# Kernel tuning notes

Hardware: AMD Instinct MI355X
Metric: run time of the kernel (lower is better)

The kernel has to match this reference:

```python
import jax, jax.numpy as jnp
import numpy as np

N_EMBD = 1024
N_HEAD = 16


def setup_inputs() -> dict:
    key = jax.random.key(0)
    ks = jax.random.split(key, 11)
    B, T, T2, C = 4, 2048, 1024, N_EMBD
    s = 0.02
    return {
        "x": jax.random.normal(ks[0], (B, T, C), jnp.float32),
        "enc_x": jax.random.normal(ks[1], (B, T2, C), jnp.float32),
        "Wq": jax.random.normal(ks[2], (C, C), jnp.float32) * s,
        "bq": jax.random.normal(ks[3], (C,), jnp.float32) * s,
        "Wk": jax.random.normal(ks[4], (C, C), jnp.float32) * s,
        "bk": jax.random.normal(ks[5], (C,), jnp.float32) * s,
        "Wv": jax.random.normal(ks[6], (C, C), jnp.float32) * s,
        "bv": jax.random.normal(ks[7], (C,), jnp.float32) * s,
        "Wo": jax.random.normal(ks[8], (C, C), jnp.float32) * s,
        "bo": jax.random.normal(ks[9], (C,), jnp.float32) * s,
    }


def reference(x, enc_x, Wq, bq, Wk, bk, Wv, bv, Wo, bo):
    B, T, C = x.shape
    B2, T2, C2 = enc_x.shape
    H = N_HEAD
    D = C // H  # head dim
    q = x @ Wq + bq          # [B,T,C]
    k = enc_x @ Wk + bk      # [B,T2,C]
    v = enc_x @ Wv + bv      # [B,T2,C]
    q = q.reshape(B, T, H, D).transpose(0, 2, 1, 3)    # [B,H,T,D]
    k = k.reshape(B2, T2, H, D).transpose(0, 2, 1, 3)  # [B,H,T2,D]
    v = v.reshape(B2, T2, H, D).transpose(0, 2, 1, 3)  # [B,H,T2,D]
    att = jnp.einsum("bhtd,bhsd->bhts", q, k) * (1.0 / jnp.sqrt(jnp.float32(D)))
    att = jax.nn.softmax(att, axis=-1)                 # [B,H,T,T2]
    y = jnp.einsum("bhts,bhsd->bhtd", att, v)          # [B,H,T,D]
    y = y.transpose(0, 2, 1, 3).reshape(B, T, C)
    return y @ Wo + bo
```

## Files before the change

### kernel.cpp

```cpp
#include <hip/hip_runtime.h>
#include <hip/hip_bf16.h>


typedef __bf16 bf16_t;
typedef __bf16 bf16x8 __attribute__((ext_vector_type(8)));
typedef float f32x4 __attribute__((ext_vector_type(4)));
typedef float f32x16 __attribute__((ext_vector_type(16)));
typedef unsigned int u32x4 __attribute__((ext_vector_type(4)));

#define AS1C(p) ((const __attribute__((address_space(1))) void*)(p))
#define AS3(p)  ((__attribute__((address_space(3))) void*)(p))

constexpr int CC  = 1024;
constexpr int TT  = 2048;
constexpr int TT2 = 1024;

#if __has_builtin(__builtin_amdgcn_exp2f)
__device__ __forceinline__ float EXP2(float x) { return __builtin_amdgcn_exp2f(x); }
#else
__device__ __forceinline__ float EXP2(float x) { return exp2f(x); }
#endif

__global__ void cast2(const float* __restrict__ in0, bf16_t* __restrict__ out0, int n0,
                      const float* __restrict__ in1, bf16_t* __restrict__ out1, int n1) {
    int i = blockIdx.x * blockDim.x + threadIdx.x;
    int stride = gridDim.x * blockDim.x;
    for (; i < n0 + n1; i += stride) {
        const float* in = (i < n0) ? in0 : in1;
        bf16_t* out = (i < n0) ? out0 : out1;
        int j = (i < n0) ? i : i - n0;
        const float4* p = (const float4*)in + 2 * (size_t)j;
        float4 a = p[0], b = p[1];
        bf16x8 v;
        v[0] = (bf16_t)a.x; v[1] = (bf16_t)a.y; v[2] = (bf16_t)a.z; v[3] = (bf16_t)a.w;
        v[4] = (bf16_t)b.x; v[5] = (bf16_t)b.y; v[6] = (bf16_t)b.z; v[7] = (bf16_t)b.w;
        *(bf16x8*)(out + (size_t)j * 8) = v;
    }
}

__global__ __launch_bounds__(256) void transW(const float* __restrict__ W0, const float* __restrict__ W1,
                                              const float* __restrict__ W2, const float* __restrict__ W3,
                                              bf16_t* __restrict__ T0, bf16_t* __restrict__ T1,
                                              bf16_t* __restrict__ T2, bf16_t* __restrict__ T3) {
    __shared__ float tile[32][33];
    const float* W; bf16_t* Tt;
    switch (blockIdx.z) {
        case 0:  W = W0; Tt = T0; break;
        case 1:  W = W1; Tt = T1; break;
        case 2:  W = W2; Tt = T2; break;
        default: W = W3; Tt = T3; break;
    }
    int x = threadIdx.x & 31, y = threadIdx.x >> 5;
    int bx = blockIdx.x * 32, by = blockIdx.y * 32;
    for (int i = 0; i < 4; ++i) {
        int r = y + i * 8;
        tile[r][x] = W[(size_t)(by + r) * 1024 + bx + x];
    }
    __syncthreads();
    for (int i = 0; i < 4; ++i) {
        int r = y + i * 8;
        Tt[(size_t)(bx + r) * 1024 + by + x] = (bf16_t)tile[x][r];
    }
}


#define SB0 __builtin_amdgcn_sched_barrier(0)
#define GLL(src, dst) __builtin_amdgcn_global_load_lds(AS1C(src), AS3(dst), 16, 0, 0)

__device__ __forceinline__ bf16x8 ldx(const char* p) { return *(const bf16x8*)p; }

__global__ __launch_bounds__(512, 2) void gemm_qkv8(const bf16_t* __restrict__ xb,
                                                    const bf16_t* __restrict__ eb,
                                                    const bf16_t* __restrict__ wtq,
                                                    const bf16_t* __restrict__ wtk,
                                                    const float* __restrict__ bq,
                                                    const float* __restrict__ bk,
                                                    const float* __restrict__ bv,
                                                    bf16_t* __restrict__ Qs,
                                                    bf16_t* __restrict__ Ks,
                                                    bf16_t* __restrict__ Vs,
                                                    float qscale) {
    __shared__ __align__(16) char GLDS[131072];
    char* ldsA = &GLDS[0];
    char* ldsB = &GLDS[65536];

    const int tid = threadIdx.x;
    const int w   = tid >> 6;
    const int l   = tid & 63;
    const int wm  = w >> 2;
    const int wn  = w & 3;
    const int l15 = l & 15, lhi = l >> 4;

    const int bid = blockIdx.x;
    const bf16_t* Ap; const bf16_t* Bp;
    int m0, n0;
    float scale;
    const float* bias; bf16_t* outp; int outn0;
    if (bid < 128) {
        int xcd = bid & 7, j = bid >> 3;
        n0 = (j & 3) * 256; m0 = (xcd * 4 + (j >> 2)) * 256;
        Ap = xb; Bp = wtq; scale = qscale;
        bias = bq; outp = Qs; outn0 = n0;
    } else {
        int b2 = bid - 128;
        int xcd = b2 & 7, j = b2 >> 3;
        n0 = (j & 7) * 256; m0 = (xcd * 2 + (j >> 3)) * 256;
        Ap = eb; Bp = wtk; scale = 1.0f;
        if (n0 < 1024) { bias = bk; outp = Ks; outn0 = n0; }
        else           { bias = bv; outp = Vs; outn0 = n0 - 1024; }
    }

    const int lrow  = l >> 3;
    const int lslot = (l & 7) ^ lrow;
    const char* Asrc = (const char*)(Ap + (size_t)(m0 + w * 16 + lrow) * 1024 + lslot * 8);
    const char* Bsrc = (const char*)(Bp + (size_t)(n0 + w * 16 + lrow) * 1024 + lslot * 8);
    #define STG_A(t, buf, h)                                                                   \
        do {                                                                                   \
            GLL(Asrc + (size_t)(h) * 262144 + (t) * 128,         ldsA + (buf) * 32768 + (h) * 16384 + w * 2048);        \
            GLL(Asrc + (size_t)(h) * 262144 + 16384 + (t) * 128, ldsA + (buf) * 32768 + (h) * 16384 + w * 2048 + 1024); \
        } while (0)
    #define STG_B(t, buf, h)                                                                   \
        do {                                                                                   \
            GLL(Bsrc + (size_t)(h) * 262144 + (t) * 128,         ldsB + (buf) * 32768 + (h) * 16384 + w * 2048);        \
            GLL(Bsrc + (size_t)(h) * 262144 + 16384 + (t) * 128, ldsB + (buf) * 32768 + (h) * 16384 + w * 2048 + 1024); \
        } while (0)

    const int aoff = (wm * 128 + l15) * 128;
    const int boff = (wn * 64 + l15) * 128;
    const int sl0  = ((0 + lhi) ^ (l15 & 7)) << 4;
    const int sl1  = ((4 + lhi) ^ (l15 & 7)) << 4;

    #define RD_A(dst, KA, qm)                                                    \
        do { _Pragma("unroll") for (int mf = 0; mf < 4; ++mf) {                  \
            dst[mf * 2 + 0] = ldx((KA) + aoff + ((qm) * 64 + mf * 16) * 128 + sl0); \
            dst[mf * 2 + 1] = ldx((KA) + aoff + ((qm) * 64 + mf * 16) * 128 + sl1); } } while (0)
    #define RD_B(dst, KB, qn)                                                    \
        do { _Pragma("unroll") for (int nf = 0; nf < 2; ++nf) {                  \
            dst[nf * 2 + 0] = ldx((KB) + boff + ((qn) * 32 + nf * 16) * 128 + sl0); \
            dst[nf * 2 + 1] = ldx((KB) + boff + ((qn) * 32 + nf * 16) * 128 + sl1); } } while (0)

    #define MFMA16(qm, qn, Af, Bf)                                                             \
        do { __builtin_amdgcn_s_setprio(1);                                                    \
            _Pragma("unroll") for (int mf = 0; mf < 4; ++mf)                                   \
            _Pragma("unroll") for (int nf = 0; nf < 2; ++nf) {                                 \
                acc[(qm) * 4 + mf][(qn) * 2 + nf] = __builtin_amdgcn_mfma_f32_16x16x32_bf16(   \
                    Af[mf * 2 + 0], Bf[nf * 2 + 0], acc[(qm) * 4 + mf][(qn) * 2 + nf], 0, 0, 0); \
                acc[(qm) * 4 + mf][(qn) * 2 + nf] = __builtin_amdgcn_mfma_f32_16x16x32_bf16(   \
                    Af[mf * 2 + 1], Bf[nf * 2 + 1], acc[(qm) * 4 + mf][(qn) * 2 + nf], 0, 0, 0); } \
            __builtin_amdgcn_s_setprio(0); } while (0)

    #define PH_BAR do { SB0; __builtin_amdgcn_s_barrier(); SB0;                                \
                        asm volatile("s_waitcnt lgkmcnt(0)" ::: "memory"); SB0; } while (0)
    #define PH_END do { SB0; __builtin_amdgcn_s_barrier(); SB0; } while (0)

    f32x4 acc[8][4] = {};
    bf16x8 A0[8], A1[8], B0[4], B1[4];

    STG_A(0, 0, 0); STG_A(0, 0, 1);
    STG_B(0, 0, 0); STG_B(0, 0, 1);
    STG_A(1, 1, 0); STG_A(1, 1, 1);
    asm volatile("s_waitcnt vmcnt(4)" ::: "memory");
    SB0; __builtin_amdgcn_s_barrier(); SB0;

    constexpr int NT = 16;
    for (int t = 0; t < NT; ++t) {
        const int buf = t & 1;
        const char* KA = ldsA + buf * 32768;
        const char* KB = ldsB + buf * 32768;

        if (t + 1 < NT) STG_B(t + 1, buf ^ 1, 0);
        RD_A(A0, KA, 0); RD_B(B0, KB, 0);
        PH_BAR;
        MFMA16(0, 0, A0, B0);
        PH_END;

        if (t + 1 < NT) STG_B(t + 1, buf ^ 1, 1);
        RD_A(A1, KA, 1);
        PH_BAR;
        MFMA16(1, 0, A1, B0);
        PH_END;

        if (t + 2 < NT) STG_A(t + 2, buf, 0);
        RD_B(B1, KB, 1);
        PH_BAR;
        MFMA16(1, 1, A1, B1);
        PH_END;

        if (t + 2 < NT) STG_A(t + 2, buf, 1);
        SB0; __builtin_amdgcn_s_barrier(); SB0;
        MFMA16(0, 1, A0, B1);
        if (t < NT - 2) asm volatile("s_waitcnt vmcnt(4)" ::: "memory");
        else            asm volatile("s_waitcnt vmcnt(0)" ::: "memory");
        PH_END;
    }

    #pragma unroll
    for (int ni = 0; ni < 4; ++ni) {
        int col = outn0 + wn * 64 + ni * 16 + l15;
        float bvv = bias[col];
        #pragma unroll
        for (int mi = 0; mi < 8; ++mi) {
            int rowb = m0 + wm * 128 + mi * 16 + lhi * 4;
            #pragma unroll
            for (int r = 0; r < 4; ++r)
                outp[(size_t)(rowb + r) * 1024 + col] = (bf16_t)((acc[mi][ni][r] + bvv) * scale);
        }
    }
    #undef STG_A
    #undef STG_B
    #undef RD_A
    #undef RD_B
    #undef MFMA16
    #undef PH_BAR
    #undef PH_END
}

__device__ __forceinline__ void gemm_body(bf16_t* As, bf16_t* Bs,
                                          const bf16_t* __restrict__ A,
                                          const bf16_t* __restrict__ Bt,
                                          const float* __restrict__ bias,
                                          float* __restrict__ out,
                                          int lgNT, int mband, int bid) {
    const int tid  = threadIdx.x;
    const int lane = tid & 63;
    const int wave = tid >> 6;
    const int wr = wave >> 1, wc = wave & 1;
    const int l15 = lane & 15, lhi = lane >> 4;

    const int xcd = bid & 7;
    const int j   = bid >> 3;
    const int n0  = (j & ((1 << lgNT) - 1)) * 128;
    const int m0  = (xcd * mband + (j >> lgNT)) * 128;

    f32x4 acc[4][4] = {};

    for (int k0 = 0; k0 < 1024; k0 += 32) {
        for (int i = 0; i < 2; ++i) {
            int e   = i * 2048 + wave * 512 + lane * 8;
            int row = e >> 5, col = e & 31;
            __builtin_amdgcn_global_load_lds(AS1C(A  + (size_t)(m0 + row) * 1024 + k0 + col),
                                             AS3(As + i * 2048 + wave * 512), 16, 0, 0);
            __builtin_amdgcn_global_load_lds(AS1C(Bt + (size_t)(n0 + row) * 1024 + k0 + col),
                                             AS3(Bs + i * 2048 + wave * 512), 16, 0, 0);
        }
        __syncthreads();
        bf16x8 a[4], b[4];
        #pragma unroll
        for (int m = 0; m < 4; ++m)
            a[m] = *(const bf16x8*)&As[(wr * 64 + m * 16 + l15) * 32 + lhi * 8];
        #pragma unroll
        for (int n = 0; n < 4; ++n)
            b[n] = *(const bf16x8*)&Bs[(wc * 64 + n * 16 + l15) * 32 + lhi * 8];
        #pragma unroll
        for (int m = 0; m < 4; ++m)
            #pragma unroll
            for (int n = 0; n < 4; ++n)
                acc[m][n] = __builtin_amdgcn_mfma_f32_16x16x32_bf16(a[m], b[n], acc[m][n], 0, 0, 0);
        __syncthreads();
    }

    #pragma unroll
    for (int n = 0; n < 4; ++n) {
        int col = n0 + wc * 64 + n * 16 + l15;
        float bv = bias[col];
        #pragma unroll
        for (int m = 0; m < 4; ++m) {
            int rowb = m0 + wr * 64 + m * 16 + lhi * 4;
            #pragma unroll
            for (int r = 0; r < 4; ++r)
                out[(size_t)(rowb + r) * 1024 + col] = acc[m][n][r] + bv;
        }
    }
}

__global__ __launch_bounds__(256) void gemm_out(const bf16_t* __restrict__ yb,
                                                const bf16_t* __restrict__ wto,
                                                const float* __restrict__ bo,
                                                float* __restrict__ out) {
    __shared__ __align__(16) bf16_t As[128 * 32];
    __shared__ __align__(16) bf16_t Bs[128 * 32];
    gemm_body(As, Bs, yb, wto, bo, out, 3, 8, blockIdx.x);
}

__global__ __launch_bounds__(256) void vtrans(const bf16_t* __restrict__ Vs, bf16_t* __restrict__ Vt) {
    __shared__ bf16_t t[64][72];
    int bh = blockIdx.y, b = bh >> 4, h = bh & 15;
    int kv0 = blockIdx.x * 64;
    int r = threadIdx.x >> 2, c0 = (threadIdx.x & 3) * 16;
    const bf16_t* src = Vs + (size_t)(b * 1024 + kv0 + r) * 1024 + h * 64 + c0;
    *(bf16x8*)&t[r][c0]     = *(const bf16x8*)src;
    *(bf16x8*)&t[r][c0 + 8] = *(const bf16x8*)(src + 8);
    __syncthreads();
    int d = threadIdx.x >> 2, k0 = (threadIdx.x & 3) * 16;
    bf16x8 v0, v1;
    #pragma unroll
    for (int j = 0; j < 8; ++j) { v0[j] = t[k0 + j][d]; v1[j] = t[k0 + 8 + j][d]; }
    bf16_t* dst = Vt + ((size_t)bh * 64 + d) * 1024 + kv0 + k0;
    *(bf16x8*)dst       = v0;
    *(bf16x8*)(dst + 8) = v1;
}

__device__ __forceinline__ unsigned pk_bf16(float lo, float hi) {
    unsigned r;
    asm("v_cvt_pk_bf16_f32 %0, %1, %2" : "=v"(r) : "v"(lo), "v"(hi));
    return r;
}
__device__ __forceinline__ void swap32(unsigned &a, unsigned &b) {
    asm("v_permlane32_swap_b32 %0, %1" : "+v"(a), "+v"(b));
}
__device__ __forceinline__ float sum_halves(float x) {
    unsigned a = __builtin_bit_cast(unsigned, x), b = a;
    swap32(a, b);
    return __builtin_bit_cast(float, a) + __builtin_bit_cast(float, b);
}
__device__ __forceinline__ bf16x8 ldsf(const bf16_t* base, int row, int colb) {
    int off = row * 128 + (colb ^ ((row & 7) << 4));
    return *(const bf16x8*)((const char*)base + off);
}
__device__ __forceinline__ bf16x8 packP(const f32x16& s0, const f32x16& s1, int kt) {
    const f32x16& sp = (kt < 2) ? s0 : s1;
    const int rb = (kt & 1) * 8;
    unsigned a0 = pk_bf16(sp[rb + 0], sp[rb + 1]);
    unsigned a1 = pk_bf16(sp[rb + 2], sp[rb + 3]);
    unsigned a2 = pk_bf16(sp[rb + 4], sp[rb + 5]);
    unsigned a3 = pk_bf16(sp[rb + 6], sp[rb + 7]);
    swap32(a0, a2);
    swap32(a1, a3);
    union { u32x4 u; bf16x8 h; } cv;
    cv.u = (u32x4){a0, a1, a2, a3};
    return cv.h;
}

__global__ __launch_bounds__(256, 2) void attn256(const bf16_t* __restrict__ Q,
                                                  const bf16_t* __restrict__ K,
                                                  const bf16_t* __restrict__ Vt,
                                                  bf16_t* __restrict__ Y) {
    __shared__ __align__(16) bf16_t SM[3][2][64 * 64];

    const int tid = threadIdx.x;
    const int l   = tid & 63;
    const int w   = tid >> 6;
    const int l31 = l & 31;
    const int lh  = l >> 5;

    const int bid = blockIdx.x;
    const int bh  = bid & 63;
    const int qb  = bid >> 6;
    const int b = bh >> 4, h = bh & 15;
    const int q0 = qb * 256 + w * 64;

    const bf16_t* Qb = Q + (size_t)b * TT * CC + h * 64;
    const char* Kc = (const char*)(K + (size_t)b * TT2 * CC + h * 64);
    const char* Vc = (const char*)(Vt + (size_t)bh * 64 * 1024);

    bf16x8 qfA[4], qfB[4];
    #pragma unroll
    for (int kt = 0; kt < 4; ++kt) {
        qfA[kt] = *(const bf16x8*)&Qb[(size_t)(q0 + l31)      * CC + kt * 16 + lh * 8];
        qfB[kt] = *(const bf16x8*)&Qb[(size_t)(q0 + 32 + l31) * CC + kt * 16 + lh * 8];
    }
    __builtin_amdgcn_sched_barrier(0);

    f32x16 yA0 = {}, yA1 = {}, yB0 = {}, yB1 = {};
    float lsA = 0.f, lsB = 0.f;

    const int krow = w * 16 + (l >> 3);
    const int ss   = ((l & 7) ^ (l >> 3)) & 7;
    const int off0 = krow * 2048 + ss * 16;
    const int off1 = off0 + 8 * 2048;

    #define STAGE(t, buf)                                                                 \
        do {                                                                              \
            __builtin_amdgcn_global_load_lds(AS1C(Kc + (size_t)(t) * 131072 + off0),      \
                                             AS3((char*)&SM[buf][0][0] + w * 2048), 16, 0, 0);        \
            __builtin_amdgcn_global_load_lds(AS1C(Kc + (size_t)(t) * 131072 + off1),      \
                                             AS3((char*)&SM[buf][0][0] + w * 2048 + 1024), 16, 0, 0); \
            __builtin_amdgcn_global_load_lds(AS1C(Vc + (t) * 128 + off0),                 \
                                             AS3((char*)&SM[buf][1][0] + w * 2048), 16, 0, 0);        \
            __builtin_amdgcn_global_load_lds(AS1C(Vc + (t) * 128 + off1),                 \
                                             AS3((char*)&SM[buf][1][0] + w * 2048 + 1024), 16, 0, 0); \
        } while (0)

    #define SUMEXP(s0, s1, ls)                                                    \
        do {                                                                      \
            float rs = 0.f;                                                       \
            _Pragma("unroll")                                                     \
            for (int r = 0; r < 16; ++r) {                                        \
                s0[r] = EXP2(s0[r]);                                              \
                s1[r] = EXP2(s1[r]);                                              \
                rs += s0[r] + s1[r];                                              \
            }                                                                     \
            ls += sum_halves(rs);                                                 \
        } while (0)

    constexpr int NT = TT2 / 64;
    STAGE(0, 0);
    STAGE(1, 1);

    int cur = 0;
    for (int t = 0; t < NT; ++t) {
        if (t + 1 < NT) asm volatile("s_waitcnt vmcnt(4)" ::: "memory");
        else            asm volatile("s_waitcnt vmcnt(0)" ::: "memory");
        __builtin_amdgcn_sched_barrier(0);
        __builtin_amdgcn_s_barrier();
        __builtin_amdgcn_sched_barrier(0);

        if (t + 2 < NT) {
            int nb = cur + 2; if (nb >= 3) nb -= 3;
            STAGE(t + 2, nb);
        }

        const bf16_t* Kl = &SM[cur][0][0];
        const bf16_t* Vl = &SM[cur][1][0];

        f32x16 sA0 = {}, sA1 = {}, sB0 = {}, sB1 = {};
        #pragma unroll
        for (int kt = 0; kt < 4; ++kt) {
            int colb = kt * 32 + (lh << 4);
            bf16x8 a0 = ldsf(Kl, l31,      colb);
            bf16x8 a1 = ldsf(Kl, 32 + l31, colb);
            sA0 = __builtin_amdgcn_mfma_f32_32x32x16_bf16(a0, qfA[kt], sA0, 0, 0, 0);
            sB0 = __builtin_amdgcn_mfma_f32_32x32x16_bf16(a0, qfB[kt], sB0, 0, 0, 0);
            sA1 = __builtin_amdgcn_mfma_f32_32x32x16_bf16(a1, qfA[kt], sA1, 0, 0, 0);
            sB1 = __builtin_amdgcn_mfma_f32_32x32x16_bf16(a1, qfB[kt], sB1, 0, 0, 0);
        }

        SUMEXP(sA0, sA1, lsA);
        SUMEXP(sB0, sB1, lsB);

        __builtin_amdgcn_s_setprio(1);
        #pragma unroll
        for (int kt = 0; kt < 4; ++kt) {
            bf16x8 pA = packP(sA0, sA1, kt);
            bf16x8 pB = packP(sB0, sB1, kt);
            int colb = kt * 32 + (lh << 4);
            bf16x8 v0 = ldsf(Vl, l31,      colb);
            bf16x8 v1 = ldsf(Vl, 32 + l31, colb);
            yA0 = __builtin_amdgcn_mfma_f32_32x32x16_bf16(v0, pA, yA0, 0, 0, 0);
            yA1 = __builtin_amdgcn_mfma_f32_32x32x16_bf16(v1, pA, yA1, 0, 0, 0);
            yB0 = __builtin_amdgcn_mfma_f32_32x32x16_bf16(v0, pB, yB0, 0, 0, 0);
            yB1 = __builtin_amdgcn_mfma_f32_32x32x16_bf16(v1, pB, yB1, 0, 0, 0);
        }
        __builtin_amdgcn_s_setprio(0);

        ++cur; if (cur == 3) cur = 0;
    }
    #undef STAGE
    #undef SUMEXP

    __syncthreads();

    float iA = 1.f / lsA, iB = 1.f / lsB;
    char* ob = (char*)&SM[0][0][0] + w * 8192;
    const int sw = (l31 & 7) << 4;
    #pragma unroll
    for (int r = 0; r < 16; ++r) {
        int drow = (r & 3) + 8 * (r >> 2) + 4 * lh;
        *(bf16_t*)(ob + l31 * 128 + ((drow * 2) ^ sw))               = (bf16_t)(yA0[r] * iA);
        *(bf16_t*)(ob + l31 * 128 + (((32 + drow) * 2) ^ sw))        = (bf16_t)(yA1[r] * iA);
        *(bf16_t*)(ob + 4096 + l31 * 128 + ((drow * 2) ^ sw))        = (bf16_t)(yB0[r] * iB);
        *(bf16_t*)(ob + 4096 + l31 * 128 + (((32 + drow) * 2) ^ sw)) = (bf16_t)(yB1[r] * iB);
    }
    __syncthreads();
    bf16_t* Yb = Y + (size_t)b * TT * CC + h * 64 + (size_t)q0 * CC;
    #pragma unroll
    for (int i = 0; i < 8; ++i) {
        int qr = i * 8 + (l >> 3);
        int c  = ((l & 7) * 16) ^ ((qr & 7) << 4);
        bf16x8 v = *(const bf16x8*)(ob + (qr >> 5) * 4096 + (qr & 31) * 128 + c);
        *(bf16x8*)&Yb[(size_t)qr * CC + (l & 7) * 8] = v;
    }
}

extern "C" void kernel_launch(void* const* d_in, const int* in_sizes, int n_in,
                              void* d_out, int out_size, void* d_ws, size_t ws_size,
                              hipStream_t stream) {
    const float* x   = (const float*)d_in[0];
    const float* enc = (const float*)d_in[1];
    const float* Wq  = (const float*)d_in[2];
    const float* bq  = (const float*)d_in[3];
    const float* Wk  = (const float*)d_in[4];
    const float* bk  = (const float*)d_in[5];
    const float* Wv  = (const float*)d_in[6];
    const float* bv  = (const float*)d_in[7];
    const float* Wo  = (const float*)d_in[8];
    const float* bo  = (const float*)d_in[9];

    char* w = (char*)d_ws;
    size_t o = 0;
    bf16_t* xb  = (bf16_t*)(w + o); o += (size_t)8192 * 1024 * 2;
    bf16_t* eb  = (bf16_t*)(w + o); o += (size_t)4096 * 1024 * 2;
    bf16_t* wtq = (bf16_t*)(w + o); o += (size_t)1024 * 1024 * 2;
    bf16_t* wtk = (bf16_t*)(w + o); o += (size_t)1024 * 1024 * 2;
    bf16_t* wtv = (bf16_t*)(w + o); o += (size_t)1024 * 1024 * 2;
    bf16_t* wto = (bf16_t*)(w + o); o += (size_t)1024 * 1024 * 2;
    bf16_t* Qs  = (bf16_t*)(w + o); o += (size_t)8192 * 1024 * 2;
    bf16_t* Ks  = (bf16_t*)(w + o); o += (size_t)4096 * 1024 * 2;
    bf16_t* Vs  = (bf16_t*)(w + o); o += (size_t)4096 * 1024 * 2;
    bf16_t* yb  = (bf16_t*)(w + o); o += (size_t)8192 * 1024 * 2;
    bf16_t* Vt  = eb;

    cast2<<<2048, 256, 0, stream>>>(x, xb, 8192 * 1024 / 8, enc, eb, 4096 * 1024 / 8);
    transW<<<dim3(32, 32, 4), 256, 0, stream>>>(Wq, Wk, Wv, Wo, wtq, wtk, wtv, wto);

    const float qscale = 0.125f * 1.4426950408889634f;
    gemm_qkv8<<<256, 512, 0, stream>>>(xb, eb, wtq, wtk, bq, bk, bv, Qs, Ks, Vs, qscale);

    vtrans<<<dim3(16, 64), 256, 0, stream>>>(Vs, Vt);

    attn256<<<512, 256, 0, stream>>>(Qs, Ks, Vt, yb);

    gemm_out<<<512, 256, 0, stream>>>(yb, wto, bo, (float*)d_out);
}
```

Before: 127.7 us.

## Fuse V transpose into QKV GEMM epilogue and merge prep kernels

The QKV GEMM epilogue now stages its output tile through LDS and writes it back with 16-byte vector stores. For the V columns it writes a per-head transposed layout directly, which removes the separate vtrans kernel and its extra read/write pass over V. The cast and weight-transpose kernels are merged into a single prep launch to save one kernel launch. The LDS staging adds a barrier and extra LDS traffic to the epilogue, and the swizzled scalar bf16 LDS writes may cause bank conflicts.

```diff
diff --git a/kernel.cpp b/kernel.cpp
--- a/kernel.cpp
+++ b/kernel.cpp
@@ -21,45 +21,50 @@
 __device__ __forceinline__ float EXP2(float x) { return exp2f(x); }
 #endif
 
-__global__ void cast2(const float* __restrict__ in0, bf16_t* __restrict__ out0, int n0,
-                      const float* __restrict__ in1, bf16_t* __restrict__ out1, int n1) {
-    int i = blockIdx.x * blockDim.x + threadIdx.x;
-    int stride = gridDim.x * blockDim.x;
-    for (; i < n0 + n1; i += stride) {
-        const float* in = (i < n0) ? in0 : in1;
-        bf16_t* out = (i < n0) ? out0 : out1;
-        int j = (i < n0) ? i : i - n0;
-        const float4* p = (const float4*)in + 2 * (size_t)j;
-        float4 a = p[0], b = p[1];
-        bf16x8 v;
-        v[0] = (bf16_t)a.x; v[1] = (bf16_t)a.y; v[2] = (bf16_t)a.z; v[3] = (bf16_t)a.w;
-        v[4] = (bf16_t)b.x; v[5] = (bf16_t)b.y; v[6] = (bf16_t)b.z; v[7] = (bf16_t)b.w;
-        *(bf16x8*)(out + (size_t)j * 8) = v;
-    }
-}
-
-__global__ __launch_bounds__(256) void transW(const float* __restrict__ W0, const float* __restrict__ W1,
-                                              const float* __restrict__ W2, const float* __restrict__ W3,
-                                              bf16_t* __restrict__ T0, bf16_t* __restrict__ T1,
-                                              bf16_t* __restrict__ T2, bf16_t* __restrict__ T3) {
+__global__ __launch_bounds__(256) void prep(const float* __restrict__ x, bf16_t* __restrict__ xb,
+                                            const float* __restrict__ enc, bf16_t* __restrict__ eb,
+                                            const float* __restrict__ W0, const float* __restrict__ W1,
+                                            const float* __restrict__ W2, const float* __restrict__ W3,
+                                            bf16_t* __restrict__ T0, bf16_t* __restrict__ T1,
+                                            bf16_t* __restrict__ T2, bf16_t* __restrict__ T3) {
     __shared__ float tile[32][33];
-    const float* W; bf16_t* Tt;
-    switch (blockIdx.z) {
-        case 0:  W = W0; Tt = T0; break;
-        case 1:  W = W1; Tt = T1; break;
-        case 2:  W = W2; Tt = T2; break;
-        default: W = W3; Tt = T3; break;
-    }
-    int x = threadIdx.x & 31, y = threadIdx.x >> 5;
-    int bx = blockIdx.x * 32, by = blockIdx.y * 32;
-    for (int i = 0; i < 4; ++i) {
-        int r = y + i * 8;
-        tile[r][x] = W[(size_t)(by + r) * 1024 + bx + x];
-    }
-    __syncthreads();
-    for (int i = 0; i < 4; ++i) {
-        int r = y + i * 8;
-        Tt[(size_t)(bx + r) * 1024 + by + x] = (bf16_t)tile[x][r];
+    const int bid = blockIdx.x;
+    if (bid < 2048) {
+        int t = bid * 256 + threadIdx.x;
+        #pragma unroll
+        for (int k = 0; k < 3; ++k) {
+            int i = t + k * 524288;
+            const float* in; bf16_t* out; int j;
+            if (i < 1048576) { in = x;   out = xb; j = i; }
+            else             { in = enc; out = eb; j = i - 1048576; }
+            const float4* p = (const float4*)in + 2 * (size_t)j;
+            float4 a = p[0], b = p[1];
+            bf16x8 v;
+            v[0] = (bf16_t)a.x; v[1] = (bf16_t)a.y; v[2] = (bf16_t)a.z; v[3] = (bf16_t)a.w;
+            v[4] = (bf16_t)b.x; v[5] = (bf16_t)b.y; v[6] = (bf16_t)b.z; v[7] = (bf16_t)b.w;
+            *(bf16x8*)(out + (size_t)j * 8) = v;
+        }
+    } else {
+        int idx = bid - 2048;
+        int bx = idx & 31, by = (idx >> 5) & 31, bz = idx >> 10;
+        const float* W; bf16_t* Tt;
+        switch (bz) {
+            case 0:  W = W0; Tt = T0; break;
+            case 1:  W = W1; Tt = T1; break;
+            case 2:  W = W2; Tt = T2; break;
+            default: W = W3; Tt = T3; break;
+        }
+        int xx = threadIdx.x & 31, yy = threadIdx.x >> 5;
+        int bxe = bx * 32, bye = by * 32;
+        for (int i = 0; i < 4; ++i) {
+            int r = yy + i * 8;
+            tile[r][xx] = W[(size_t)(bye + r) * 1024 + bxe + xx];
+        }
+        __syncthreads();
+        for (int i = 0; i < 4; ++i) {
+            int r = yy + i * 8;
+            Tt[(size_t)(bxe + r) * 1024 + bye + xx] = (bf16_t)tile[xx][r];
+        }
     }
 }
 
@@ -96,6 +101,7 @@
     int m0, n0;
     float scale;
     const float* bias; bf16_t* outp; int outn0;
+    bool vout = false;
     if (bid < 128) {
         int xcd = bid & 7, j = bid >> 3;
         n0 = (j & 3) * 256; m0 = (xcd * 4 + (j >> 2)) * 256;
@@ -107,7 +113,7 @@
         n0 = (j & 7) * 256; m0 = (xcd * 2 + (j >> 3)) * 256;
         Ap = eb; Bp = wtk; scale = 1.0f;
         if (n0 < 1024) { bias = bk; outp = Ks; outn0 = n0; }
-        else           { bias = bv; outp = Vs; outn0 = n0 - 1024; }
+        else           { bias = bv; outp = Vs; outn0 = n0 - 1024; vout = true; }
     }
 
     const int lrow  = l >> 3;
@@ -194,16 +200,61 @@
         PH_END;
     }
 
-    #pragma unroll
-    for (int ni = 0; ni < 4; ++ni) {
-        int col = outn0 + wn * 64 + ni * 16 + l15;
-        float bvv = bias[col];
-        #pragma unroll
-        for (int mi = 0; mi < 8; ++mi) {
-            int rowb = m0 + wm * 128 + mi * 16 + lhi * 4;
+    __syncthreads();
+    char* EP = GLDS + w * 16384;
+
+    if (!vout) {
+        #pragma unroll
+        for (int ni = 0; ni < 4; ++ni) {
+            int c_rel = ni * 16 + l15;
+            float bvv = bias[outn0 + wn * 64 + c_rel];
             #pragma unroll
-            for (int r = 0; r < 4; ++r)
-                outp[(size_t)(rowb + r) * 1024 + col] = (bf16_t)((acc[mi][ni][r] + bvv) * scale);
+            for (int mi = 0; mi < 8; ++mi) {
+                int mbase = mi * 16 + lhi * 4;
+                #pragma unroll
+                for (int r = 0; r < 4; ++r)
+                    *(bf16_t*)(EP + (mbase + r) * 128 + c_rel * 2) =
+                        (bf16_t)((acc[mi][ni][r] + bvv) * scale);
+            }
+        }
+        asm volatile("s_waitcnt lgkmcnt(0)" ::: "memory");
+        SB0;
+        char* gbase = (char*)outp + (size_t)(m0 + wm * 128) * 2048 + (outn0 + wn * 64) * 2;
+        #pragma unroll
+        for (int i = 0; i < 16; ++i) {
+            int m_rel = i * 8 + (l >> 3);
+            int ch = l & 7;
+            bf16x8 v = *(const bf16x8*)(EP + m_rel * 128 + ch * 16);
+            *(bf16x8*)(gbase + (size_t)m_rel * 2048 + ch * 16) = v;
+        }
+    } else {
+        int col0 = outn0 + wn * 64;
+        int hh = col0 >> 6;
+        int rowbase = m0 + wm * 128;
+        int bb = rowbase >> 10, key0 = rowbase & 1023;
+        #pragma unroll
+        for (int ni = 0; ni < 4; ++ni) {
+            int dd = ni * 16 + l15;
+            float bvv = bias[col0 + dd];
+            int sw = (dd & 7) << 4;
+            #pragma unroll
+            for (int mi = 0; mi < 8; ++mi) {
+                int kb = mi * 16 + lhi * 4;
+                #pragma unroll
+                for (int r = 0; r < 4; ++r)
+                    *(bf16_t*)(EP + dd * 256 + (((kb + r) * 2) ^ sw)) =
+                        (bf16_t)((acc[mi][ni][r] + bvv) * scale);
+            }
+        }
+        asm volatile("s_waitcnt lgkmcnt(0)" ::: "memory");
+        SB0;
+        char* gbase = (char*)outp + ((size_t)((bb * 16 + hh) * 64) * 1024 + key0) * 2;
+        #pragma unroll
+        for (int i = 0; i < 16; ++i) {
+            int dd = i * 4 + (l >> 4);
+            int ch = l & 15;
+            bf16x8 v = *(const bf16x8*)(EP + dd * 256 + ((ch * 16) ^ ((dd & 7) << 4)));
+            *(bf16x8*)(gbase + (size_t)dd * 2048 + ch * 16) = v;
         }
     }
     #undef STG_A
@@ -280,24 +331,6 @@
     __shared__ __align__(16) bf16_t As[128 * 32];
     __shared__ __align__(16) bf16_t Bs[128 * 32];
     gemm_body(As, Bs, yb, wto, bo, out, 3, 8, blockIdx.x);
-}
-
-__global__ __launch_bounds__(256) void vtrans(const bf16_t* __restrict__ Vs, bf16_t* __restrict__ Vt) {
-    __shared__ bf16_t t[64][72];
-    int bh = blockIdx.y, b = bh >> 4, h = bh & 15;
-    int kv0 = blockIdx.x * 64;
-    int r = threadIdx.x >> 2, c0 = (threadIdx.x & 3) * 16;
-    const bf16_t* src = Vs + (size_t)(b * 1024 + kv0 + r) * 1024 + h * 64 + c0;
-    *(bf16x8*)&t[r][c0]     = *(const bf16x8*)src;
-    *(bf16x8*)&t[r][c0 + 8] = *(const bf16x8*)(src + 8);
-    __syncthreads();
-    int d = threadIdx.x >> 2, k0 = (threadIdx.x & 3) * 16;
-    bf16x8 v0, v1;
-    #pragma unroll
-    for (int j = 0; j < 8; ++j) { v0[j] = t[k0 + j][d]; v1[j] = t[k0 + 8 + j][d]; }
-    bf16_t* dst = Vt + ((size_t)bh * 64 + d) * 1024 + kv0 + k0;
-    *(bf16x8*)dst       = v0;
-    *(bf16x8*)(dst + 8) = v1;
 }
 
 __device__ __forceinline__ unsigned pk_bf16(float lo, float hi) {
@@ -496,17 +529,13 @@
     bf16_t* wto = (bf16_t*)(w + o); o += (size_t)1024 * 1024 * 2;
     bf16_t* Qs  = (bf16_t*)(w + o); o += (size_t)8192 * 1024 * 2;
     bf16_t* Ks  = (bf16_t*)(w + o); o += (size_t)4096 * 1024 * 2;
-    bf16_t* Vs  = (bf16_t*)(w + o); o += (size_t)4096 * 1024 * 2;
+    bf16_t* Vt  = (bf16_t*)(w + o); o += (size_t)4096 * 1024 * 2;
     bf16_t* yb  = (bf16_t*)(w + o); o += (size_t)8192 * 1024 * 2;
-    bf16_t* Vt  = eb;
-
-    cast2<<<2048, 256, 0, stream>>>(x, xb, 8192 * 1024 / 8, enc, eb, 4096 * 1024 / 8);
-    transW<<<dim3(32, 32, 4), 256, 0, stream>>>(Wq, Wk, Wv, Wo, wtq, wtk, wtv, wto);
+
+    prep<<<6144, 256, 0, stream>>>(x, xb, enc, eb, Wq, Wk, Wv, Wo, wtq, wtk, wtv, wto);
 
     const float qscale = 0.125f * 1.4426950408889634f;
-    gemm_qkv8<<<256, 512, 0, stream>>>(xb, eb, wtq, wtk, bq, bk, bv, Qs, Ks, Vs, qscale);
-
-    vtrans<<<dim3(16, 64), 256, 0, stream>>>(Vs, Vt);
+    gemm_qkv8<<<256, 512, 0, stream>>>(xb, eb, wtq, wtk, bq, bk, bv, Qs, Ks, Vt, qscale);
 
     attn256<<<512, 256, 0, stream>>>(Qs, Ks, Vt, yb);
 
```

Result: faster. 118.7 us (-7.1%).
